# Kernel tuning notes

Hardware: AMD Instinct MI355X
Metric: run time of the kernel (lower is better)

The kernel has to match this reference:

```python
import jax, jax.numpy as jnp
import numpy as np

PI = float(np.pi)

def setup_inputs() -> dict:
    key = jax.random.key(0)
    # Pixel-like values in [0, 255)
    inputs = jax.random.uniform(key, (32768, 3, 32, 32), dtype=jnp.float32) * 255.0
    return {"inputs": inputs}

def reference(inputs) -> jnp.ndarray:
    B = inputs.shape[0]
    # 4x4 average pooling per channel, then channel mean -> [B, 8, 8]
    patches = inputs.reshape(B, 3, 8, 8, 4, 4).mean(axis=(-1, -2)).mean(axis=1)
    angles = patches.reshape(B, -1) / 255.0 * PI - PI / 2.0  # [B, 64]
    # RY(theta) on |0>, then <Z> = cos(theta) exactly (no entangling gates)
    return jnp.cos(angles)
```

## Files before the change

kernel.cpp:

```cpp
#include <hip/hip_runtime.h>

#define PI_F 3.14159265358979323846f

__global__ __launch_bounds__(256) void qa_pool_cos_kernel(
    const float* __restrict__ in, float* __restrict__ out, int total)
{
    int idx = blockIdx.x * blockDim.x + threadIdx.x;
    if (idx >= total) return;

    int b = idx >> 6;
    int p = idx & 63;

    const float* base = in + (size_t)b * 3072 + p * 16;

    float s = 0.0f;
#pragma unroll
    for (int c = 0; c < 3; ++c) {
        const float4* cb = reinterpret_cast<const float4*>(base + c * 1024);
#pragma unroll
        for (int q = 0; q < 4; ++q) {
            float4 v = cb[q];
            s += (v.x + v.y) + (v.z + v.w);
        }
    }

    float patch = s * (1.0f / 48.0f);
    float ang   = patch * (PI_F / 255.0f) - (PI_F * 0.5f);
    out[idx] = __cosf(ang);
}

extern "C" void kernel_launch(void* const* d_in, const int* in_sizes, int n_in,
                              void* d_out, int out_size, void* d_ws, size_t ws_size,
                              hipStream_t stream) {
    const float* in  = (const float*)d_in[0];
    float*       out = (float*)d_out;

    int total = out_size;
    int block = 256;
    int grid  = (total + block - 1) / block;

    qa_pool_cos_kernel<<<grid, block, 0, stream>>>(in, out, total);
}
```

Baseline: 511.7 us.

## Assign one block per image with coalesced float4 loads and shuffle reduction

Launches one 768-thread block per image, so each thread loads a single consecutive float4 and adjacent threads read adjacent memory. Before, each thread read 16 strided floats itself. Groups of four lanes sum their patch with xor shuffles and write per-channel partial sums to shared memory. After a barrier, 64 threads combine the three channels and apply the cosine. This aims to fix poorly coalesced loads on a bandwidth-bound kernel, at the cost of a block barrier and only 64 active threads in the final stage.

```diff
diff --git a/kernel.cpp b/kernel.cpp
--- a/kernel.cpp
+++ b/kernel.cpp
@@ -2,42 +2,40 @@
 
 #define PI_F 3.14159265358979323846f
 
-__global__ __launch_bounds__(256) void qa_pool_cos_kernel(
-    const float* __restrict__ in, float* __restrict__ out, int total)
+__global__ __launch_bounds__(768) void qa_pool_cos_kernel(
+    const float4* __restrict__ in4, float* __restrict__ out)
 {
-    int idx = blockIdx.x * blockDim.x + threadIdx.x;
-    if (idx >= total) return;
+    __shared__ float partial[192];
 
-    int b = idx >> 6;
-    int p = idx & 63;
+    int b   = blockIdx.x;
+    int tid = threadIdx.x;
 
-    const float* base = in + (size_t)b * 3072 + p * 16;
+    float4 v = in4[(size_t)b * 768 + tid];
+    float s = (v.x + v.y) + (v.z + v.w);
 
-    float s = 0.0f;
-#pragma unroll
-    for (int c = 0; c < 3; ++c) {
-        const float4* cb = reinterpret_cast<const float4*>(base + c * 1024);
-#pragma unroll
-        for (int q = 0; q < 4; ++q) {
-            float4 v = cb[q];
-            s += (v.x + v.y) + (v.z + v.w);
-        }
+    s += __shfl_xor(s, 1, 64);
+    s += __shfl_xor(s, 2, 64);
+
+    if ((tid & 3) == 0) {
+        int c = tid >> 8;
+        int p = (tid & 255) >> 2;
+        partial[c * 64 + p] = s;
     }
+    __syncthreads();
 
-    float patch = s * (1.0f / 48.0f);
-    float ang   = patch * (PI_F / 255.0f) - (PI_F * 0.5f);
-    out[idx] = __cosf(ang);
+    if (tid < 64) {
+        float total = partial[tid] + partial[64 + tid] + partial[128 + tid];
+        float ang   = total * (1.0f / 48.0f) * (PI_F / 255.0f) - (PI_F * 0.5f);
+        out[(size_t)b * 64 + tid] = __cosf(ang);
+    }
 }
 
 extern "C" void kernel_launch(void* const* d_in, const int* in_sizes, int n_in,
                               void* d_out, int out_size, void* d_ws, size_t ws_size,
                               hipStream_t stream) {
-    const float* in  = (const float*)d_in[0];
-    float*       out = (float*)d_out;
+    const float4* in4 = (const float4*)d_in[0];
+    float*        out = (float*)d_out;
 
-    int total = out_size;
-    int block = 256;
-    int grid  = (total + block - 1) / block;
-
-    qa_pool_cos_kernel<<<grid, block, 0, stream>>>(in, out, total);
+    int B = out_size / 64;
+    qa_pool_cos_kernel<<<B, 768, 0, stream>>>(in4, out);
 }
```

Result: no change. 502.7 us (-1.8%).
